# Kernel tuning notes

Hardware: AMD Instinct MI355X
Metric: run time of the kernel (lower is better)

Reference implementation:

```python
import jax, jax.numpy as jnp
import numpy as np

N_NODES = 10000
N_EDGES = 320000
T = 24
H = 64


def setup_inputs() -> dict:
    key = jax.random.key(0)
    ks = jax.random.split(key, 16)
    s = 0.1  # keep LSTM gates in a sane range
    return {
        "blob": jax.random.normal(ks[0], (N_NODES, T), dtype=jnp.float32),
        "W_ih": s * jax.random.normal(ks[1], (N_NODES, 4 * H, 1), dtype=jnp.float32),
        "b_ih": s * jax.random.normal(ks[2], (N_NODES, 4 * H), dtype=jnp.float32),
        "W_hh": s * jax.random.normal(ks[3], (N_NODES, 4 * H, H), dtype=jnp.float32),
        "b_hh": s * jax.random.normal(ks[4], (N_NODES, 4 * H), dtype=jnp.float32),
        "Wg0": s * jax.random.normal(ks[5], (H, H), dtype=jnp.float32),
        "bg0": s * jax.random.normal(ks[6], (H,), dtype=jnp.float32),
        "Wg1": s * jax.random.normal(ks[7], (H, H), dtype=jnp.float32),
        "bg1": s * jax.random.normal(ks[8], (H,), dtype=jnp.float32),
        "Wg2": s * jax.random.normal(ks[9], (H, 1), dtype=jnp.float32),
        "bg2": s * jax.random.normal(ks[10], (1,), dtype=jnp.float32),
        "edge_src": jax.random.randint(ks[11], (N_EDGES,), 0, N_NODES, dtype=jnp.int32),
        "edge_dst": jax.random.randint(ks[12], (N_EDGES,), 0, N_NODES, dtype=jnp.int32),
    }


def _sym_norms(edge_src, edge_dst, n, dtype):
    ones = jnp.ones(edge_src.shape[0], dtype=dtype)
    deg_out = jax.ops.segment_sum(ones, edge_src, num_segments=n)
    deg_in = jax.ops.segment_sum(ones, edge_dst, num_segments=n)
    inv_sqrt = lambda d: jnp.where(d > 0, jnp.where(d > 0, d, 1.0) ** -0.5, 0.0)
    return inv_sqrt(deg_out), inv_sqrt(deg_in)


def reference(blob, W_ih, b_ih, W_hh, b_hh, Wg0, bg0, Wg1, bg1, Wg2, bg2,
              edge_src, edge_dst):
    n = blob.shape[0]
    norm_src, norm_dst = _sym_norms(edge_src, edge_dst, n, blob.dtype)

    def gconv(h, W, b, act=None):
        # DGL GraphConv, norm='both': D_dst^{-1/2} A D_src^{-1/2} h W + b
        msg = (h * norm_src[:, None])[edge_src]            # [E, F]
        agg = jax.ops.segment_sum(msg, edge_dst, num_segments=n)
        out = (agg * norm_dst[:, None]) @ W + b
        return act(out) if act is not None else out

    # Per-node LSTM, batched across all nodes; torch gate order i,f,g,o.
    Wx = W_ih[:, :, 0]  # [N, 4H] since in_feats == 1

    def step(carry, x_t):
        h, c = carry  # [N,H] each
        gates = (Wx * x_t[:, None] + b_ih
                 + jnp.einsum('nh,ngh->ng', h, W_hh) + b_hh)  # [N,4H]
        i, f, g, o = jnp.split(gates, 4, axis=1)
        c = jax.nn.sigmoid(f) * c + jax.nn.sigmoid(i) * jnp.tanh(g)
        h = jax.nn.sigmoid(o) * jnp.tanh(c)
        # GCN stack on current hidden states (dropout is identity at eval)
        z = gconv(h, Wg0, bg0, jax.nn.relu)
        z = gconv(z, Wg1, bg1, jax.nn.relu)
        z = gconv(z, Wg2, bg2)                               # [N,1]
        return (h, c), z[:, 0]

    h0 = jnp.zeros((n, H), dtype=blob.dtype)
    c0 = jnp.zeros((n, H), dtype=blob.dtype)
    _, ys = jax.lax.scan(step, (h0, c0), blob.T)  # ys: [T, N]
    return ys.T  # [N, T]
```

## Files before the change

kernel.cpp:

```cpp
#include <hip/hip_runtime.h>
#include <cstdint>
#include <cstddef>

#define NN 10000
#define NE 320000
#define TT 24
#define HD 64
#define G4 256

__device__ __forceinline__ float sigm(float x){ return 1.0f/(1.0f + __expf(-x)); }
__device__ __forceinline__ float tanh_fast(float x){ return 2.0f/(1.0f + __expf(-2.0f*x)) - 1.0f; }

__global__ __launch_bounds__(256) void degree_kernel(const int* __restrict__ esrc, const int* __restrict__ edst,
                                                     int* __restrict__ deg_out, int* __restrict__ deg_in){
  int e = blockIdx.x*256 + threadIdx.x;
  if (e < NE){
    atomicAdd(&deg_out[esrc[e]], 1);
    atomicAdd(&deg_in[edst[e]], 1);
  }
}

__global__ __launch_bounds__(256) void norm_kernel(const int* __restrict__ deg_out, const int* __restrict__ deg_in,
                                                   float* __restrict__ norm_src, float* __restrict__ norm_dst){
  int i = blockIdx.x*256 + threadIdx.x;
  if (i < NN){
    int a = deg_out[i]; norm_src[i] = (a>0) ? rsqrtf((float)a) : 0.0f;
    int b = deg_in[i];  norm_dst[i] = (b>0) ? rsqrtf((float)b) : 0.0f;
  }
}

__global__ __launch_bounds__(256) void scan_kernel(const int* __restrict__ deg_in, int* __restrict__ csr_off,
                                                   int* __restrict__ cursor){
  __shared__ int sums[256];
  const int CH = (NN + 255)/256;
  int tid = threadIdx.x;
  int beg = tid*CH; if (beg > NN) beg = NN;
  int end = beg+CH; if (end > NN) end = NN;
  int s = 0;
  for (int i=beg;i<end;i++) s += deg_in[i];
  sums[tid] = s;
  __syncthreads();
  if (tid == 0){
    int run = 0;
    for (int i=0;i<256;i++){ int v = sums[i]; sums[i] = run; run += v; }
  }
  __syncthreads();
  int run = sums[tid];
  for (int i=beg;i<end;i++){ csr_off[i] = run; cursor[i] = run; run += deg_in[i]; }
  if (tid == 0) csr_off[NN] = NE;
}

__global__ __launch_bounds__(256) void fill_kernel(const int* __restrict__ esrc, const int* __restrict__ edst,
                                                   int* __restrict__ cursor, int* __restrict__ csr_src,
                                                   float* __restrict__ csr_w, const float* __restrict__ norm_src){
  int e = blockIdx.x*256 + threadIdx.x;
  if (e < NE){
    int d = edst[e]; int s = esrc[e];
    int pos = atomicAdd(&cursor[d], 1);
    csr_src[pos] = s;
    csr_w[pos]   = norm_src[s];
  }
}

__global__ __launch_bounds__(256) void lstm_kernel(const float* __restrict__ blob, const float* __restrict__ W_ih,
                                                   const float* __restrict__ b_ih, const float* __restrict__ W_hh,
                                                   const float* __restrict__ b_hh, float* __restrict__ h_all){
  const int n = blockIdx.x;
  const int g = threadIdx.x;
  __shared__ float lh[HD];
  __shared__ float lg[G4];

  float4 w4[16];
  const float4* wp = reinterpret_cast<const float4*>(W_hh + (size_t)n*(G4*HD) + (size_t)g*HD);
  #pragma unroll
  for (int i=0;i<16;i++) w4[i] = wp[i];

  const float wx = W_ih[(size_t)n*G4 + g];
  const float bs = b_ih[(size_t)n*G4 + g] + b_hh[(size_t)n*G4 + g];

  float c = 0.0f;
  if (g < HD) lh[g] = 0.0f;
  __syncthreads();

  for (int t=0;t<TT;t++){
    float xt = blob[n*TT + t];
    float gate = fmaf(wx, xt, bs);
    const float4* h4 = reinterpret_cast<const float4*>(lh);
    #pragma unroll
    for (int i=0;i<16;i++){
      float4 hv = h4[i];
      gate = fmaf(hv.x, w4[i].x, gate);
      gate = fmaf(hv.y, w4[i].y, gate);
      gate = fmaf(hv.z, w4[i].z, gate);
      gate = fmaf(hv.w, w4[i].w, gate);
    }
    lg[g] = gate;
    __syncthreads();
    if (g < HD){
      float iv = sigm(lg[g]);
      float fv = sigm(lg[HD+g]);
      float gv = tanh_fast(lg[2*HD+g]);
      float ov = sigm(lg[3*HD+g]);
      c = fmaf(fv, c, iv*gv);
      float h = ov * tanh_fast(c);
      lh[g] = h;
      h_all[(size_t)n*(TT*HD) + (size_t)t*HD + g] = h;
    }
    __syncthreads();
  }
}

__global__ __launch_bounds__(256) void gconv_mid_kernel(const float* __restrict__ src_feat, float* __restrict__ dst_feat,
                                                        const float* __restrict__ Wg, const float* __restrict__ bg,
                                                        const int* __restrict__ csr_off, const int* __restrict__ csr_src,
                                                        const float* __restrict__ csr_w, const float* __restrict__ norm_dst){
  int n = blockIdx.x*4 + (threadIdx.x >> 6);
  int lane = threadIdx.x & 63;
  if (n >= NN) return;

  float wcol[HD];
  #pragma unroll
  for (int k=0;k<HD;k++) wcol[k] = Wg[k*HD + lane];
  float bias = bg[lane];

  float acc[TT];
  #pragma unroll
  for (int t=0;t<TT;t++) acc[t] = 0.0f;

  int e = csr_off[n];
  const int end = csr_off[n+1];
  for (; e < end; e++){
    int s = csr_src[e];
    float w = csr_w[e];
    const float* p = src_feat + (size_t)s*(TT*HD) + lane;
    float v[TT];
    #pragma unroll
    for (int t=0;t<TT;t++) v[t] = p[t*HD];
    #pragma unroll
    for (int t=0;t<TT;t++) acc[t] = fmaf(w, v[t], acc[t]);
  }
  float nd = norm_dst[n];
  #pragma unroll
  for (int t=0;t<TT;t++) acc[t] *= nd;

  float* dbase = dst_feat + (size_t)n*(TT*HD) + lane;
  #pragma unroll
  for (int t=0;t<TT;t++){
    float out = bias;
    #pragma unroll
    for (int k=0;k<HD;k++){
      float ak = __shfl(acc[t], k, 64);
      out = fmaf(ak, wcol[k], out);
    }
    out = fmaxf(out, 0.0f);
    dbase[t*HD] = out;
  }
}

__global__ __launch_bounds__(256) void gconv_last_kernel(const float* __restrict__ src_feat, float* __restrict__ q,
                                                         const float* __restrict__ Wg, const float* __restrict__ bg,
                                                         const float* __restrict__ Wg2,
                                                         const int* __restrict__ csr_off, const int* __restrict__ csr_src,
                                                         const float* __restrict__ csr_w, const float* __restrict__ norm_dst,
                                                         const float* __restrict__ norm_src){
  int n = blockIdx.x*4 + (threadIdx.x >> 6);
  int lane = threadIdx.x & 63;
  if (n >= NN) return;

  float wcol[HD];
  #pragma unroll
  for (int k=0;k<HD;k++) wcol[k] = Wg[k*HD + lane];
  float bias = bg[lane];
  float w2 = Wg2[lane];

  float acc[TT];
  #pragma unroll
  for (int t=0;t<TT;t++) acc[t] = 0.0f;

  int e = csr_off[n];
  const int end = csr_off[n+1];
  for (; e < end; e++){
    int s = csr_src[e];
    float w = csr_w[e];
    const float* p = src_feat + (size_t)s*(TT*HD) + lane;
    float v[TT];
    #pragma unroll
    for (int t=0;t<TT;t++) v[t] = p[t*HD];
    #pragma unroll
    for (int t=0;t<TT;t++) acc[t] = fmaf(w, v[t], acc[t]);
  }
  float nd = norm_dst[n];
  #pragma unroll
  for (int t=0;t<TT;t++) acc[t] *= nd;

  float ns = norm_src[n];
  #pragma unroll
  for (int t=0;t<TT;t++){
    float out = bias;
    #pragma unroll
    for (int k=0;k<HD;k++){
      float ak = __shfl(acc[t], k, 64);
      out = fmaf(ak, wcol[k], out);
    }
    out = fmaxf(out, 0.0f);
    float p2 = out * w2;
    #pragma unroll
    for (int off=32; off; off >>= 1) p2 += __shfl_xor(p2, off, 64);
    if (lane == 0) q[n*32 + t] = p2 * ns;
  }
}

__global__ __launch_bounds__(256) void out_kernel(const float* __restrict__ q, const int* __restrict__ csr_off,
                                                  const int* __restrict__ csr_src, const float* __restrict__ norm_dst,
                                                  const float* __restrict__ bg2, float* __restrict__ out){
  int wid = blockIdx.x*4 + (threadIdx.x >> 6);
  int lane = threadIdx.x & 63;
  if (wid >= NN) return;
  int n = wid;
  int e = csr_off[n];
  const int end = csr_off[n+1];
  if (lane < TT){
    float s0 = 0.f, s1 = 0.f, s2 = 0.f, s3 = 0.f;
    for (; e+3 < end; e += 4){
      int a = csr_src[e], b = csr_src[e+1], c = csr_src[e+2], d = csr_src[e+3];
      s0 += q[a*32 + lane];
      s1 += q[b*32 + lane];
      s2 += q[c*32 + lane];
      s3 += q[d*32 + lane];
    }
    for (; e < end; e++) s0 += q[csr_src[e]*32 + lane];
    float s = (s0+s1)+(s2+s3);
    out[n*TT + lane] = fmaf(norm_dst[n], s, bg2[0]);
  }
}

extern "C" void kernel_launch(void* const* d_in, const int* in_sizes, int n_in,
                              void* d_out, int out_size, void* d_ws, size_t ws_size,
                              hipStream_t stream) {
  (void)in_sizes; (void)n_in; (void)out_size; (void)ws_size;
  const float* blob  = (const float*)d_in[0];
  const float* W_ih  = (const float*)d_in[1];
  const float* b_ih  = (const float*)d_in[2];
  const float* W_hh  = (const float*)d_in[3];
  const float* b_hh  = (const float*)d_in[4];
  const float* Wg0   = (const float*)d_in[5];
  const float* bg0   = (const float*)d_in[6];
  const float* Wg1   = (const float*)d_in[7];
  const float* bg1   = (const float*)d_in[8];
  const float* Wg2   = (const float*)d_in[9];
  const float* bg2   = (const float*)d_in[10];
  const int* edge_src = (const int*)d_in[11];
  const int* edge_dst = (const int*)d_in[12];
  float* out = (float*)d_out;

  char* ws = (char*)d_ws;
  size_t off = 0;
  auto alloc = [&](size_t bytes)->char* {
    char* p = ws + off; off += (bytes + 255) & ~(size_t)255; return p;
  };
  float* h_all   = (float*)alloc((size_t)TT*NN*HD*sizeof(float));
  float* z1      = (float*)alloc((size_t)TT*NN*HD*sizeof(float));
  float* q       = (float*)alloc((size_t)NN*32*sizeof(float));
  int*   deg_out = (int*)  alloc((size_t)NN*sizeof(int));
  int*   deg_in  = (int*)  alloc((size_t)NN*sizeof(int));
  float* norm_src= (float*)alloc((size_t)NN*sizeof(float));
  float* norm_dst= (float*)alloc((size_t)NN*sizeof(float));
  int*   csr_off = (int*)  alloc((size_t)(NN+1)*sizeof(int));
  int*   cursor  = (int*)  alloc((size_t)NN*sizeof(int));
  int*   csr_src = (int*)  alloc((size_t)NE*sizeof(int));
  float* csr_w   = (float*)alloc((size_t)NE*sizeof(float));

  hipMemsetAsync(deg_out, 0, (size_t)NN*sizeof(int), stream);
  hipMemsetAsync(deg_in,  0, (size_t)NN*sizeof(int), stream);

  degree_kernel<<<(NE+255)/256, 256, 0, stream>>>(edge_src, edge_dst, deg_out, deg_in);
  norm_kernel<<<(NN+255)/256, 256, 0, stream>>>(deg_out, deg_in, norm_src, norm_dst);
  scan_kernel<<<1, 256, 0, stream>>>(deg_in, csr_off, cursor);
  fill_kernel<<<(NE+255)/256, 256, 0, stream>>>(edge_src, edge_dst, cursor, csr_src, csr_w, norm_src);

  lstm_kernel<<<NN, 256, 0, stream>>>(blob, W_ih, b_ih, W_hh, b_hh, h_all);

  gconv_mid_kernel<<<(NN+3)/4, 256, 0, stream>>>(h_all, z1, Wg0, bg0, csr_off, csr_src, csr_w, norm_dst);
  gconv_last_kernel<<<(NN+3)/4, 256, 0, stream>>>(z1, q, Wg1, bg1, Wg2, csr_off, csr_src, csr_w, norm_dst, norm_src);
  out_kernel<<<(NN+3)/4, 256, 0, stream>>>(q, csr_off, csr_src, norm_dst, bg2, out);
}
```

Before: 1.648 ms.

## Store intermediate features as fp16 pairs and split GCN gather across two warps per node

The LSTM hidden states and the first GCN layer output are now stored in fp16, with pairs of timesteps packed into half2, which halves the bytes moved by the edge-gather in both GCN kernels. Each node is handled by two warps, each covering six timestep pairs. The edge loop is unrolled by two, and CSR source index and weight are packed into one int2 array. The output kernel now splits edges across half-waves. The cost is reduced intermediate precision, which may add error relative to the fp32 reference, plus more redundant loads of the weight matrix because twice as many warps are launched.

```diff
diff --git a/kernel.cpp b/kernel.cpp
--- a/kernel.cpp
+++ b/kernel.cpp
@@ -1,10 +1,12 @@
 #include <hip/hip_runtime.h>
+#include <hip/hip_fp16.h>
 #include <cstdint>
 #include <cstddef>
 
 #define NN 10000
 #define NE 320000
 #define TT 24
+#define TP 12
 #define HD 64
 #define G4 256
 
@@ -51,20 +53,19 @@
 }
 
 __global__ __launch_bounds__(256) void fill_kernel(const int* __restrict__ esrc, const int* __restrict__ edst,
-                                                   int* __restrict__ cursor, int* __restrict__ csr_src,
-                                                   float* __restrict__ csr_w, const float* __restrict__ norm_src){
+                                                   int* __restrict__ cursor, int2* __restrict__ csr_pk,
+                                                   const float* __restrict__ norm_src){
   int e = blockIdx.x*256 + threadIdx.x;
   if (e < NE){
     int d = edst[e]; int s = esrc[e];
     int pos = atomicAdd(&cursor[d], 1);
-    csr_src[pos] = s;
-    csr_w[pos]   = norm_src[s];
+    csr_pk[pos] = make_int2(s, __float_as_int(norm_src[s]));
   }
 }
 
 __global__ __launch_bounds__(256) void lstm_kernel(const float* __restrict__ blob, const float* __restrict__ W_ih,
                                                    const float* __restrict__ b_ih, const float* __restrict__ W_hh,
-                                                   const float* __restrict__ b_hh, float* __restrict__ h_all){
+                                                   const float* __restrict__ b_hh, __half* __restrict__ h_all){
   const int n = blockIdx.x;
   const int g = threadIdx.x;
   __shared__ float lh[HD];
@@ -104,134 +105,203 @@
       c = fmaf(fv, c, iv*gv);
       float h = ov * tanh_fast(c);
       lh[g] = h;
-      h_all[(size_t)n*(TT*HD) + (size_t)t*HD + g] = h;
+      h_all[(((size_t)n*TP + (t>>1))*HD + g)*2 + (t&1)] = __float2half(h);
     }
     __syncthreads();
   }
 }
 
-__global__ __launch_bounds__(256) void gconv_mid_kernel(const float* __restrict__ src_feat, float* __restrict__ dst_feat,
+__global__ __launch_bounds__(256) void gconv_mid_kernel(const __half2* __restrict__ src_feat, __half2* __restrict__ dst_feat,
                                                         const float* __restrict__ Wg, const float* __restrict__ bg,
-                                                        const int* __restrict__ csr_off, const int* __restrict__ csr_src,
-                                                        const float* __restrict__ csr_w, const float* __restrict__ norm_dst){
+                                                        const int* __restrict__ csr_off, const int2* __restrict__ csr_pk,
+                                                        const float* __restrict__ norm_dst){
+  int wid = blockIdx.x*4 + (threadIdx.x >> 6);
+  int lane = threadIdx.x & 63;
+  if (wid >= NN*2) return;
+  int n  = wid >> 1;
+  int hf = wid & 1;
+  const int tpo = hf*6;
+
+  float wcol[HD];
+  #pragma unroll
+  for (int k=0;k<HD;k++) wcol[k] = Wg[k*HD + lane];
+  float bias = bg[lane];
+
+  float2 acc[6];
+  #pragma unroll
+  for (int j=0;j<6;j++) acc[j] = make_float2(0.f, 0.f);
+
+  int e = csr_off[n];
+  const int end = csr_off[n+1];
+  for (; e+1 < end; e += 2){
+    int2 p0 = csr_pk[e];
+    int2 p1 = csr_pk[e+1];
+    float w0 = __int_as_float(p0.y);
+    float w1 = __int_as_float(p1.y);
+    const __half2* b0 = src_feat + (size_t)p0.x*(TP*HD) + tpo*HD + lane;
+    const __half2* b1 = src_feat + (size_t)p1.x*(TP*HD) + tpo*HD + lane;
+    __half2 u0[6], u1[6];
+    #pragma unroll
+    for (int j=0;j<6;j++) u0[j] = b0[j*HD];
+    #pragma unroll
+    for (int j=0;j<6;j++) u1[j] = b1[j*HD];
+    #pragma unroll
+    for (int j=0;j<6;j++){
+      float2 f0 = __half22float2(u0[j]);
+      float2 f1 = __half22float2(u1[j]);
+      acc[j].x = fmaf(w0, f0.x, acc[j].x);
+      acc[j].y = fmaf(w0, f0.y, acc[j].y);
+      acc[j].x = fmaf(w1, f1.x, acc[j].x);
+      acc[j].y = fmaf(w1, f1.y, acc[j].y);
+    }
+  }
+  if (e < end){
+    int2 p0 = csr_pk[e];
+    float w0 = __int_as_float(p0.y);
+    const __half2* b0 = src_feat + (size_t)p0.x*(TP*HD) + tpo*HD + lane;
+    #pragma unroll
+    for (int j=0;j<6;j++){
+      float2 f0 = __half22float2(b0[j*HD]);
+      acc[j].x = fmaf(w0, f0.x, acc[j].x);
+      acc[j].y = fmaf(w0, f0.y, acc[j].y);
+    }
+  }
+  float nd = norm_dst[n];
+  #pragma unroll
+  for (int j=0;j<6;j++){ acc[j].x *= nd; acc[j].y *= nd; }
+
+  __half2* dbase = dst_feat + (size_t)n*(TP*HD) + tpo*HD + lane;
+  #pragma unroll
+  for (int j=0;j<6;j++){
+    float oe = bias, oo = bias;
+    #pragma unroll
+    for (int k=0;k<HD;k++){
+      float ae = __shfl(acc[j].x, k, 64);
+      float ao = __shfl(acc[j].y, k, 64);
+      oe = fmaf(ae, wcol[k], oe);
+      oo = fmaf(ao, wcol[k], oo);
+    }
+    oe = fmaxf(oe, 0.0f);
+    oo = fmaxf(oo, 0.0f);
+    dbase[j*HD] = __floats2half2_rn(oe, oo);
+  }
+}
+
+__global__ __launch_bounds__(256) void gconv_last_kernel(const __half2* __restrict__ src_feat, float* __restrict__ q,
+                                                         const float* __restrict__ Wg, const float* __restrict__ bg,
+                                                         const float* __restrict__ Wg2,
+                                                         const int* __restrict__ csr_off, const int2* __restrict__ csr_pk,
+                                                         const float* __restrict__ norm_dst, const float* __restrict__ norm_src){
+  int wid = blockIdx.x*4 + (threadIdx.x >> 6);
+  int lane = threadIdx.x & 63;
+  if (wid >= NN*2) return;
+  int n  = wid >> 1;
+  int hf = wid & 1;
+  const int tpo = hf*6;
+
+  float wcol[HD];
+  #pragma unroll
+  for (int k=0;k<HD;k++) wcol[k] = Wg[k*HD + lane];
+  float bias = bg[lane];
+  float w2 = Wg2[lane];
+
+  float2 acc[6];
+  #pragma unroll
+  for (int j=0;j<6;j++) acc[j] = make_float2(0.f, 0.f);
+
+  int e = csr_off[n];
+  const int end = csr_off[n+1];
+  for (; e+1 < end; e += 2){
+    int2 p0 = csr_pk[e];
+    int2 p1 = csr_pk[e+1];
+    float w0 = __int_as_float(p0.y);
+    float w1 = __int_as_float(p1.y);
+    const __half2* b0 = src_feat + (size_t)p0.x*(TP*HD) + tpo*HD + lane;
+    const __half2* b1 = src_feat + (size_t)p1.x*(TP*HD) + tpo*HD + lane;
+    __half2 u0[6], u1[6];
+    #pragma unroll
+    for (int j=0;j<6;j++) u0[j] = b0[j*HD];
+    #pragma unroll
+    for (int j=0;j<6;j++) u1[j] = b1[j*HD];
+    #pragma unroll
+    for (int j=0;j<6;j++){
+      float2 f0 = __half22float2(u0[j]);
+      float2 f1 = __half22float2(u1[j]);
+      acc[j].x = fmaf(w0, f0.x, acc[j].x);
+      acc[j].y = fmaf(w0, f0.y, acc[j].y);
+      acc[j].x = fmaf(w1, f1.x, acc[j].x);
+      acc[j].y = fmaf(w1, f1.y, acc[j].y);
+    }
+  }
+  if (e < end){
+    int2 p0 = csr_pk[e];
+    float w0 = __int_as_float(p0.y);
+    const __half2* b0 = src_feat + (size_t)p0.x*(TP*HD) + tpo*HD + lane;
+    #pragma unroll
+    for (int j=0;j<6;j++){
+      float2 f0 = __half22float2(b0[j*HD]);
+      acc[j].x = fmaf(w0, f0.x, acc[j].x);
+      acc[j].y = fmaf(w0, f0.y, acc[j].y);
+    }
+  }
+  float nd = norm_dst[n];
+  #pragma unroll
+  for (int j=0;j<6;j++){ acc[j].x *= nd; acc[j].y *= nd; }
+
+  float ns = norm_src[n];
+  #pragma unroll
+  for (int j=0;j<6;j++){
+    float oe = bias, oo = bias;
+    #pragma unroll
+    for (int k=0;k<HD;k++){
+      float ae = __shfl(acc[j].x, k, 64);
+      float ao = __shfl(acc[j].y, k, 64);
+      oe = fmaf(ae, wcol[k], oe);
+      oo = fmaf(ao, wcol[k], oo);
+    }
+    oe = fmaxf(oe, 0.0f) * w2;
+    oo = fmaxf(oo, 0.0f) * w2;
+    #pragma unroll
+    for (int off=32; off; off >>= 1){
+      oe += __shfl_xor(oe, off, 64);
+      oo += __shfl_xor(oo, off, 64);
+    }
+    if (lane == 0){
+      int tp = tpo + j;
+      q[n*32 + 2*tp]     = oe * ns;
+      q[n*32 + 2*tp + 1] = oo * ns;
+    }
+  }
+}
+
+__global__ __launch_bounds__(256) void out_kernel(const float* __restrict__ q, const int* __restrict__ csr_off,
+                                                  const int2* __restrict__ csr_pk, const float* __restrict__ norm_dst,
+                                                  const float* __restrict__ bg2, float* __restrict__ out){
   int n = blockIdx.x*4 + (threadIdx.x >> 6);
   int lane = threadIdx.x & 63;
   if (n >= NN) return;
-
-  float wcol[HD];
-  #pragma unroll
-  for (int k=0;k<HD;k++) wcol[k] = Wg[k*HD + lane];
-  float bias = bg[lane];
-
-  float acc[TT];
-  #pragma unroll
-  for (int t=0;t<TT;t++) acc[t] = 0.0f;
-
+  int sub = lane >> 5;
+  int tl  = lane & 31;
+  bool act = tl < TT;
   int e = csr_off[n];
   const int end = csr_off[n+1];
-  for (; e < end; e++){
-    int s = csr_src[e];
-    float w = csr_w[e];
-    const float* p = src_feat + (size_t)s*(TT*HD) + lane;
-    float v[TT];
-    #pragma unroll
-    for (int t=0;t<TT;t++) v[t] = p[t*HD];
-    #pragma unroll
-    for (int t=0;t<TT;t++) acc[t] = fmaf(w, v[t], acc[t]);
-  }
-  float nd = norm_dst[n];
-  #pragma unroll
-  for (int t=0;t<TT;t++) acc[t] *= nd;
-
-  float* dbase = dst_feat + (size_t)n*(TT*HD) + lane;
-  #pragma unroll
-  for (int t=0;t<TT;t++){
-    float out = bias;
-    #pragma unroll
-    for (int k=0;k<HD;k++){
-      float ak = __shfl(acc[t], k, 64);
-      out = fmaf(ak, wcol[k], out);
-    }
-    out = fmaxf(out, 0.0f);
-    dbase[t*HD] = out;
-  }
-}
-
-__global__ __launch_bounds__(256) void gconv_last_kernel(const float* __restrict__ src_feat, float* __restrict__ q,
-                                                         const float* __restrict__ Wg, const float* __restrict__ bg,
-                                                         const float* __restrict__ Wg2,
-                                                         const int* __restrict__ csr_off, const int* __restrict__ csr_src,
-                                                         const float* __restrict__ csr_w, const float* __restrict__ norm_dst,
-                                                         const float* __restrict__ norm_src){
-  int n = blockIdx.x*4 + (threadIdx.x >> 6);
-  int lane = threadIdx.x & 63;
-  if (n >= NN) return;
-
-  float wcol[HD];
-  #pragma unroll
-  for (int k=0;k<HD;k++) wcol[k] = Wg[k*HD + lane];
-  float bias = bg[lane];
-  float w2 = Wg2[lane];
-
-  float acc[TT];
-  #pragma unroll
-  for (int t=0;t<TT;t++) acc[t] = 0.0f;
-
-  int e = csr_off[n];
-  const int end = csr_off[n+1];
-  for (; e < end; e++){
-    int s = csr_src[e];
-    float w = csr_w[e];
-    const float* p = src_feat + (size_t)s*(TT*HD) + lane;
-    float v[TT];
-    #pragma unroll
-    for (int t=0;t<TT;t++) v[t] = p[t*HD];
-    #pragma unroll
-    for (int t=0;t<TT;t++) acc[t] = fmaf(w, v[t], acc[t]);
-  }
-  float nd = norm_dst[n];
-  #pragma unroll
-  for (int t=0;t<TT;t++) acc[t] *= nd;
-
-  float ns = norm_src[n];
-  #pragma unroll
-  for (int t=0;t<TT;t++){
-    float out = bias;
-    #pragma unroll
-    for (int k=0;k<HD;k++){
-      float ak = __shfl(acc[t], k, 64);
-      out = fmaf(ak, wcol[k], out);
-    }
-    out = fmaxf(out, 0.0f);
-    float p2 = out * w2;
-    #pragma unroll
-    for (int off=32; off; off >>= 1) p2 += __shfl_xor(p2, off, 64);
-    if (lane == 0) q[n*32 + t] = p2 * ns;
-  }
-}
-
-__global__ __launch_bounds__(256) void out_kernel(const float* __restrict__ q, const int* __restrict__ csr_off,
-                                                  const int* __restrict__ csr_src, const float* __restrict__ norm_dst,
-                                                  const float* __restrict__ bg2, float* __restrict__ out){
-  int wid = blockIdx.x*4 + (threadIdx.x >> 6);
-  int lane = threadIdx.x & 63;
-  if (wid >= NN) return;
-  int n = wid;
-  int e = csr_off[n];
-  const int end = csr_off[n+1];
-  if (lane < TT){
-    float s0 = 0.f, s1 = 0.f, s2 = 0.f, s3 = 0.f;
-    for (; e+3 < end; e += 4){
-      int a = csr_src[e], b = csr_src[e+1], c = csr_src[e+2], d = csr_src[e+3];
-      s0 += q[a*32 + lane];
-      s1 += q[b*32 + lane];
-      s2 += q[c*32 + lane];
-      s3 += q[d*32 + lane];
-    }
-    for (; e < end; e++) s0 += q[csr_src[e]*32 + lane];
-    float s = (s0+s1)+(s2+s3);
-    out[n*TT + lane] = fmaf(norm_dst[n], s, bg2[0]);
-  }
+  float s0 = 0.f, s1 = 0.f;
+  for (; e+3 < end; e += 4){
+    int a = csr_pk[e+sub].x;
+    int b = csr_pk[e+2+sub].x;
+    if (act){
+      s0 += q[a*32 + tl];
+      s1 += q[b*32 + tl];
+    }
+  }
+  for (; e+1 < end; e += 2){
+    int a = csr_pk[e+sub].x;
+    if (act) s0 += q[a*32 + tl];
+  }
+  if (e < end && sub == 0 && act) s1 += q[csr_pk[e].x*32 + tl];
+  float s = s0 + s1;
+  s += __shfl_xor(s, 32, 64);
+  if (sub == 0 && act) out[n*TT + tl] = fmaf(norm_dst[n], s, bg2[0]);
 }
 
 extern "C" void kernel_launch(void* const* d_in, const int* in_sizes, int n_in,
@@ -258,17 +328,16 @@
   auto alloc = [&](size_t bytes)->char* {
     char* p = ws + off; off += (bytes + 255) & ~(size_t)255; return p;
   };
-  float* h_all   = (float*)alloc((size_t)TT*NN*HD*sizeof(float));
-  float* z1      = (float*)alloc((size_t)TT*NN*HD*sizeof(float));
-  float* q       = (float*)alloc((size_t)NN*32*sizeof(float));
-  int*   deg_out = (int*)  alloc((size_t)NN*sizeof(int));
-  int*   deg_in  = (int*)  alloc((size_t)NN*sizeof(int));
-  float* norm_src= (float*)alloc((size_t)NN*sizeof(float));
-  float* norm_dst= (float*)alloc((size_t)NN*sizeof(float));
-  int*   csr_off = (int*)  alloc((size_t)(NN+1)*sizeof(int));
-  int*   cursor  = (int*)  alloc((size_t)NN*sizeof(int));
-  int*   csr_src = (int*)  alloc((size_t)NE*sizeof(int));
-  float* csr_w   = (float*)alloc((size_t)NE*sizeof(float));
+  __half* h_all   = (__half*)alloc((size_t)NN*TT*HD*sizeof(__half));
+  __half* z1      = (__half*)alloc((size_t)NN*TT*HD*sizeof(__half));
+  float*  q       = (float*) alloc((size_t)NN*32*sizeof(float));
+  int*    deg_out = (int*)   alloc((size_t)NN*sizeof(int));
+  int*    deg_in  = (int*)   alloc((size_t)NN*sizeof(int));
+  float*  norm_src= (float*) alloc((size_t)NN*sizeof(float));
+  float*  norm_dst= (float*) alloc((size_t)NN*sizeof(float));
+  int*    csr_off = (int*)   alloc((size_t)(NN+1)*sizeof(int));
+  int*    cursor  = (int*)   alloc((size_t)NN*sizeof(int));
+  int2*   csr_pk  = (int2*)  alloc((size_t)NE*sizeof(int2));
 
   hipMemsetAsync(deg_out, 0, (size_t)NN*sizeof(int), stream);
   hipMemsetAsync(deg_in,  0, (size_t)NN*sizeof(int), stream);
@@ -276,11 +345,13 @@
   degree_kernel<<<(NE+255)/256, 256, 0, stream>>>(edge_src, edge_dst, deg_out, deg_in);
   norm_kernel<<<(NN+255)/256, 256, 0, stream>>>(deg_out, deg_in, norm_src, norm_dst);
   scan_kernel<<<1, 256, 0, stream>>>(deg_in, csr_off, cursor);
-  fill_kernel<<<(NE+255)/256, 256, 0, stream>>>(edge_src, edge_dst, cursor, csr_src, csr_w, norm_src);
+  fill_kernel<<<(NE+255)/256, 256, 0, stream>>>(edge_src, edge_dst, cursor, csr_pk, norm_src);
 
   lstm_kernel<<<NN, 256, 0, stream>>>(blob, W_ih, b_ih, W_hh, b_hh, h_all);
 
-  gconv_mid_kernel<<<(NN+3)/4, 256, 0, stream>>>(h_all, z1, Wg0, bg0, csr_off, csr_src, csr_w, norm_dst);
-  gconv_last_kernel<<<(NN+3)/4, 256, 0, stream>>>(z1, q, Wg1, bg1, Wg2, csr_off, csr_src, csr_w, norm_dst, norm_src);
-  out_kernel<<<(NN+3)/4, 256, 0, stream>>>(q, csr_off, csr_src, norm_dst, bg2, out);
-}
+  gconv_mid_kernel<<<(NN*2+3)/4, 256, 0, stream>>>((const __half2*)h_all, (__half2*)z1, Wg0, bg0,
+                                                   csr_off, csr_pk, norm_dst);
+  gconv_last_kernel<<<(NN*2+3)/4, 256, 0, stream>>>((const __half2*)z1, q, Wg1, bg1, Wg2,
+                                                    csr_off, csr_pk, norm_dst, norm_src);
+  out_kernel<<<(NN+3)/4, 256, 0, stream>>>(q, csr_off, csr_pk, norm_dst, bg2, out);
+}
```

New measurement: 1.414 ms. -14.2%, faster.
